# Kernel optimization log

Measured on AMD Instinct MI355X. Metric: run time of the kernel, lower is better.

## Reference

```python
import jax, jax.numpy as jnp
from jax import lax
import numpy as np

B, C, H, W = 32, 256, 56, 56
K = 3
EPS = 1e-5


def setup_inputs() -> dict:
    key = jax.random.key(0)
    k1, k2, k3, k4 = jax.random.split(key, 4)
    x = jax.random.normal(k1, (B, C, H, W), dtype=jnp.float32)
    # xavier_normal init for conv weight [C_out, C_in, K, K]
    fan_in = C * K * K
    fan_out = C * K * K
    std = float(np.sqrt(2.0 / (fan_in + fan_out)))
    w = jax.random.normal(k2, (C, C, K, K), dtype=jnp.float32) * std
    gamma = jnp.ones((C,), dtype=jnp.float32)
    beta = jnp.zeros((C,), dtype=jnp.float32)
    return {"x": x, "w": w, "gamma": gamma, "beta": beta}


def reference(x, w, gamma, beta):
    # --- Binarize (bi_act_method=0, bi_w_scale=1) ---
    bx = jnp.sign(x)                                   # activation sign
    wc = jnp.clip(w, -1.0, 1.0)                        # fp_weight.data.clamp_(-1,1)
    mean_val = jnp.mean(jnp.abs(wc))
    bw = jnp.sign(wc) * mean_val                       # sign(w) * mean(|w|)
    # --- float conv2d, stride 1, padding 1 ---
    out = lax.conv_general_dilated(
        bx, bw, window_strides=(1, 1), padding=[(1, 1), (1, 1)],
        dimension_numbers=("NCHW", "OIHW", "NCHW"))
    # --- identity shortcut (stride=1, C_in==C_out) ---
    out = out + x
    # --- BatchNorm2d (training-mode batch stats, affine) ---
    mean = jnp.mean(out, axis=(0, 2, 3), keepdims=True)
    var = jnp.var(out, axis=(0, 2, 3), keepdims=True)
    out = (out - mean) * lax.rsqrt(var + EPS)
    out = out * gamma[None, :, None, None] + beta[None, :, None, None]
    # --- ReLU ---
    return jax.nn.relu(out)
```

## Files before the change

### kernel.cpp

```cpp
#include <hip/hip_runtime.h>
#include <cstdint>

#define Bn   32
#define Cn   256
#define Hn   56
#define Wn   56
#define HWn  (Hn*Wn)
#define NPIX (Bn*HWn)
#define WELEMS (Cn*Cn*9)
#define EPSv 1e-5f

#define PR   58
#define PPLANE (PR*PR)

#define F_WPART 8
#define F_SUM   64
#define F_SQ    320
#define WPK_OFF  4096
#define WPK_BYTES WELEMS
#define ACT_OFF  (WPK_OFF + WPK_BYTES)
#define ACT_BYTES (Bn*PPLANE*Cn)

typedef int v4i __attribute__((ext_vector_type(4)));

#define GLOBAL_AS __attribute__((address_space(1)))
#define LDS_AS    __attribute__((address_space(3)))

__global__ void pack_all(const float* __restrict__ x,
                         const float* __restrict__ w,
                         float* __restrict__ wsf,
                         uint8_t* __restrict__ wpk,
                         uint8_t* __restrict__ act) {
    if (blockIdx.x < 392) {
        if (blockIdx.x < 2)
            wsf[F_SUM + blockIdx.x * 256 + threadIdx.x] = 0.0f;

        int v = blockIdx.x * 256 + threadIdx.x;
        if (v < 7296) {
            int b = v / 228;
            int r = v - b * 228;
            int y, xx;
            if (r < 58)       { y = 0;  xx = r; }
            else if (r < 116) { y = 57; xx = r - 58; }
            else { int r2 = r - 116; y = 1 + (r2 >> 1); xx = (r2 & 1) * 57; }
            uint4* d = (uint4*)(act + ((size_t)(b * PR + y) * PR + xx) * 256);
            uint4 z = make_uint4(0, 0, 0, 0);
            #pragma unroll
            for (int i = 0; i < 16; i++) d[i] = z;
        }
        int b = v / HWn;
        int p = v - b * HWn;
        int y = p / Wn;
        int xx = p - y * Wn;
        const float* xp = x + (size_t)b * Cn * HWn + p;
        int key = (xx + 1) & 15;
        uint32_t* dst = (uint32_t*)(act + ((size_t)(b * PR + (y + 1)) * PR + (xx + 1)) * 256);
        #pragma unroll
        for (int slot = 0; slot < 16; slot++) {
            uint32_t rr[4];
            #pragma unroll
            for (int cw = 0; cw < 4; cw++) {
                uint32_t r = 0;
                #pragma unroll
                for (int j = 0; j < 4; j++) {
                    uint32_t sgn = __float_as_uint(xp[(size_t)(slot * 16 + cw * 4 + j) * HWn]) >> 31;
                    r |= (sgn ? 0xFFu : 0x01u) << (j * 8);
                }
                rr[cw] = r;
            }
            *(uint4*)(dst + (size_t)((slot ^ key) * 4)) = make_uint4(rr[0], rr[1], rr[2], rr[3]);
        }
    } else {
        int u = (blockIdx.x - 392) * 256 + threadIdx.x;
        int co = u / 36;
        int kc = u - co * 36;
        int t  = kc >> 2;
        int s  = kc & 3;
        const float* wp = w + (size_t)co * 2304 + t;
        uint32_t* dst = (uint32_t*)(wpk + ((size_t)kc * 256 + co) * 64);
        float sabs = 0.0f;
        #pragma unroll
        for (int cw = 0; cw < 16; cw++) {
            uint32_t r = 0;
            #pragma unroll
            for (int j = 0; j < 4; j++) {
                int ci = s * 64 + cw * 4 + j;
                float wv = wp[(size_t)ci * 9];
                sabs += fminf(fabsf(wv), 1.0f);
                r |= ((__float_as_uint(wv) >> 31) ? 0xFFu : 0x01u) << (j * 8);
            }
            dst[cw] = r;
        }
        #pragma unroll
        for (int off = 32; off; off >>= 1) sabs += __shfl_down(sabs, off);
        __shared__ float sh[4];
        if ((threadIdx.x & 63) == 0) sh[threadIdx.x >> 6] = sabs;
        __syncthreads();
        if (threadIdx.x == 0)
            wsf[F_WPART + (blockIdx.x - 392)] = sh[0] + sh[1] + sh[2] + sh[3];
    }
}

__global__ __launch_bounds__(256, 2) void conv_mfma(
    const uint8_t* __restrict__ act, const uint8_t* __restrict__ wpk,
    const float* __restrict__ x, float* __restrict__ wsf,
    float* __restrict__ out) {
    __shared__ uint4 ldsv[3712];
    uint8_t* lds = (uint8_t*)ldsv;

    const int tid  = threadIdx.x;
    const int lane = tid & 63;
    const int wid  = tid >> 6;
    const int l15  = lane & 15;
    const int l4   = lane >> 4;

    const int bx = blockIdx.x;
    const int b  = bx / 28;
    const int y0 = (bx - b * 28) * 2;

    {
        const uint8_t* src = act + ((size_t)b * PR + y0) * PR * 256;
        #pragma unroll
        for (int j = 0; j < 15; j++) {
            int c = wid + j * 4;
            if (c < 58) {
                __builtin_amdgcn_global_load_lds(
                    (const GLOBAL_AS uint32_t*)(const void*)(src + c * 1024 + lane * 16),
                    (LDS_AS uint32_t*)(void*)(lds + c * 1024),
                    16, 0, 0);
            }
        }
    }

    const uint8_t* abase = wpk + (wid * 64 + l15) * 64 + l4 * 16;

    v4i af0[4], af1[4], af2[4], af3[4];
    #pragma unroll
    for (int mi = 0; mi < 4; mi++) {
        af0[mi] = *(const v4i*)(abase + (size_t)0 * 16384 + mi * 1024);
        af1[mi] = *(const v4i*)(abase + (size_t)1 * 16384 + mi * 1024);
        af2[mi] = *(const v4i*)(abase + (size_t)2 * 16384 + mi * 1024);
        af3[mi] = *(const v4i*)(abase + (size_t)3 * 16384 + mi * 1024);
    }

    int pixb[7], key[7];
    #pragma unroll
    for (int ni = 0; ni < 7; ni++) {
        int n  = ni * 16 + l15;
        int r_ = n / 56;
        int c_ = n - r_ * 56;
        pixb[ni] = (r_ * 58 + c_) * 256;
        key[ni]  = c_ & 15;
    }

    __syncthreads();

    v4i acc[4][7] = {};

#define STEP(S, AF)                                                            \
    {                                                                          \
        v4i bf[7];                                                             \
        _Pragma("unroll")                                                      \
        for (int ni = 0; ni < 7; ni++)                                         \
            bf[ni] = *(const v4i*)(lds + pixb[ni] +                            \
                                   ((((S) * 4 + l4) ^ key[ni]) << 4));         \
        _Pragma("unroll")                                                      \
        for (int ni = 0; ni < 7; ni++) {                                       \
            _Pragma("unroll")                                                  \
            for (int mi = 0; mi < 4; mi++)                                     \
                acc[mi][ni] = __builtin_amdgcn_mfma_i32_16x16x64_i8(           \
                    AF[mi], bf[ni], acc[mi][ni], 0, 0, 0);                     \
        }                                                                      \
        {                                                                      \
            int kcn = t4 + (S) + 4;                                            \
            kcn = kcn > 35 ? 35 : kcn;     \
            const uint8_t* ap = abase + (size_t)kcn * 16384;                   \
            _Pragma("unroll")                                                  \
            for (int mi = 0; mi < 4; mi++)                                     \
                AF[mi] = *(const v4i*)(ap + mi * 1024);                        \
        }                                                                      \
    }

    #pragma unroll 1
    for (int t = 0; t < 9; t++) {
        const int t4 = t * 4;
        STEP(0, af0)
        STEP(1, af1)
        STEP(2, af2)
        STEP(3, af3)
        const int wrap  = (t == 2 || t == 5);
        const int dtoff = (t == 8) ? 0 : (wrap ? 56 * 256 : 256);
        const int ddw   = (t == 8) ? 0 : (wrap ? -2 : 1);
        #pragma unroll
        for (int ni = 0; ni < 7; ni++) {
            pixb[ni] += dtoff;
            key[ni]   = (key[ni] + ddw) & 15;
        }
    }
#undef STEP

    float wabs = 0.0f;
    #pragma unroll
    for (int j = 0; j < 36; j++) wabs += wsf[F_WPART + j];
    const float mv = wabs * (1.0f / (float)WELEMS);

    const int co_w = wid * 64;
    const int pbase = b * (Cn * HWn) + y0 * 56;

    float ssum[4][4] = {}, ssq[4][4] = {};
    #pragma unroll
    for (int mi = 0; mi < 4; mi++) {
        #pragma unroll
        for (int ni = 0; ni < 7; ni++) {
            v4i a = acc[mi][ni];
            #pragma unroll
            for (int q = 0; q < 4; q++) {
                int co = co_w + mi * 16 + l4 * 4 + q;
                size_t idx = (size_t)pbase + (size_t)co * HWn + (ni * 16 + l15);
                float val = fmaf(mv, (float)a[q], x[idx]);
                out[idx] = val;
                ssum[mi][q] += val;
                ssq[mi][q]  += val * val;
            }
        }
    }
    #pragma unroll
    for (int mi = 0; mi < 4; mi++) {
        #pragma unroll
        for (int q = 0; q < 4; q++) {
            float s = ssum[mi][q], sq = ssq[mi][q];
            #pragma unroll
            for (int off = 1; off < 16; off <<= 1) {
                s  += __shfl_xor(s, off);
                sq += __shfl_xor(sq, off);
            }
            if (l15 == 0) {
                int co = co_w + mi * 16 + l4 * 4 + q;
                atomicAdd(&wsf[F_SUM + co], s);
                atomicAdd(&wsf[F_SQ  + co], sq);
            }
        }
    }
}

__global__ void epilogue_kernel(float* __restrict__ out,
                                const float* __restrict__ wsf,
                                const float* __restrict__ g,
                                const float* __restrict__ bt) {
    int plane = blockIdx.x;
    int c = plane & 255;
    const float n = (float)(Bn * HWn);
    float mean = wsf[F_SUM + c] / n;
    float var  = wsf[F_SQ + c] / n - mean * mean;
    float sc = g[c] * rsqrtf(var + EPSv);
    float sh = bt[c] - mean * sc;
    float4* o4 = (float4*)(out + (size_t)plane * HWn);
    for (int i = threadIdx.x; i < HWn / 4; i += 256) {
        float4 v = o4[i];
        v.x = fmaxf(fmaf(v.x, sc, sh), 0.0f);
        v.y = fmaxf(fmaf(v.y, sc, sh), 0.0f);
        v.z = fmaxf(fmaf(v.z, sc, sh), 0.0f);
        v.w = fmaxf(fmaf(v.w, sc, sh), 0.0f);
        o4[i] = v;
    }
}

extern "C" void kernel_launch(void* const* d_in, const int* in_sizes, int n_in,
                              void* d_out, int out_size, void* d_ws, size_t ws_size,
                              hipStream_t stream) {
    const float* x     = (const float*)d_in[0];
    const float* w     = (const float*)d_in[1];
    const float* gamma = (const float*)d_in[2];
    const float* beta  = (const float*)d_in[3];
    float* out = (float*)d_out;

    float*   wsf = (float*)d_ws;
    uint8_t* wpk = (uint8_t*)d_ws + WPK_OFF;
    uint8_t* act = (uint8_t*)d_ws + ACT_OFF;

    pack_all<<<dim3(428), dim3(256), 0, stream>>>(x, w, wsf, wpk, act);
    conv_mfma<<<dim3(896), dim3(256), 0, stream>>>(act, wpk, x, wsf, out);
    epilogue_kernel<<<dim3(Bn * Cn), dim3(256), 0, stream>>>(out, wsf, gamma, beta);
}
```

Baseline: 346.8 us.

## Split conv block into 8 waves, each handling half the pixel tiles

Doubles the conv block from 256 to 512 threads. Each pair of waves now shares one 64-output-channel group and splits its 7 pixel tiles into 4 and 3. Weight prefetch shrinks from four steps ahead to one step, which cuts per-thread registers (fewer accumulators and A fragments) and targets higher occupancy through launch bounds (512,4). In exchange, weight fragments are loaded twice per block, prefetch distance is shorter and latency may be exposed, and the 4/3 split leaves the two halves of each wave pair with unequal work.

```diff
diff --git a/kernel.cpp b/kernel.cpp
--- a/kernel.cpp
+++ b/kernel.cpp
@@ -101,7 +101,109 @@
     }
 }
 
-__global__ __launch_bounds__(256, 2) void conv_mfma(
+template<int NF>
+__device__ __forceinline__ void conv_body(
+    const uint8_t* lds, const uint8_t* abase,
+    const float* __restrict__ x, float* __restrict__ wsf,
+    float* __restrict__ out, float mv,
+    int f0, int l15, int l4, int co_w, int pbase) {
+
+    int pixb[NF], key[NF];
+    #pragma unroll
+    for (int ni = 0; ni < NF; ni++) {
+        int n  = (f0 + ni) * 16 + l15;
+        int r_ = n / 56;
+        int c_ = n - r_ * 56;
+        pixb[ni] = (r_ * 58 + c_) * 256;
+        key[ni]  = c_ & 15;
+    }
+
+    v4i af[4];
+    #pragma unroll
+    for (int mi = 0; mi < 4; mi++)
+        af[mi] = *(const v4i*)(abase + mi * 1024);
+
+    v4i acc[4][NF] = {};
+
+#define STEP(S)                                                                \
+    {                                                                          \
+        v4i bf[NF];                                                            \
+        _Pragma("unroll")                                                      \
+        for (int ni = 0; ni < NF; ni++)                                        \
+            bf[ni] = *(const v4i*)(lds + pixb[ni] +                            \
+                                   ((((S) * 4 + l4) ^ key[ni]) << 4));         \
+        _Pragma("unroll")                                                      \
+        for (int ni = 0; ni < NF; ni++) {                                      \
+            _Pragma("unroll")                                                  \
+            for (int mi = 0; mi < 4; mi++)                                     \
+                acc[mi][ni] = __builtin_amdgcn_mfma_i32_16x16x64_i8(           \
+                    af[mi], bf[ni], acc[mi][ni], 0, 0, 0);                     \
+        }                                                                      \
+        {                                                                      \
+            int kcn = t4 + (S) + 1;                                            \
+            kcn = kcn > 35 ? 35 : kcn;     \
+            const uint8_t* ap = abase + (size_t)kcn * 16384;                   \
+            _Pragma("unroll")                                                  \
+            for (int mi = 0; mi < 4; mi++)                                     \
+                af[mi] = *(const v4i*)(ap + mi * 1024);                        \
+        }                                                                      \
+    }
+
+    #pragma unroll 1
+    for (int t = 0; t < 9; t++) {
+        const int t4 = t * 4;
+        STEP(0)
+        STEP(1)
+        STEP(2)
+        STEP(3)
+        const int wrap  = (t == 2 || t == 5);
+        const int dtoff = (t == 8) ? 0 : (wrap ? 56 * 256 : 256);
+        const int ddw   = (t == 8) ? 0 : (wrap ? -2 : 1);
+        #pragma unroll
+        for (int ni = 0; ni < NF; ni++) {
+            pixb[ni] += dtoff;
+            key[ni]   = (key[ni] + ddw) & 15;
+        }
+    }
+#undef STEP
+
+    float ssum[4][4] = {}, ssq[4][4] = {};
+    #pragma unroll
+    for (int mi = 0; mi < 4; mi++) {
+        #pragma unroll
+        for (int ni = 0; ni < NF; ni++) {
+            v4i a = acc[mi][ni];
+            #pragma unroll
+            for (int q = 0; q < 4; q++) {
+                int co = co_w + mi * 16 + l4 * 4 + q;
+                size_t idx = (size_t)pbase + (size_t)co * HWn + ((f0 + ni) * 16 + l15);
+                float val = fmaf(mv, (float)a[q], x[idx]);
+                out[idx] = val;
+                ssum[mi][q] += val;
+                ssq[mi][q]  += val * val;
+            }
+        }
+    }
+    #pragma unroll
+    for (int mi = 0; mi < 4; mi++) {
+        #pragma unroll
+        for (int q = 0; q < 4; q++) {
+            float s = ssum[mi][q], sq = ssq[mi][q];
+            #pragma unroll
+            for (int off = 1; off < 16; off <<= 1) {
+                s  += __shfl_xor(s, off);
+                sq += __shfl_xor(sq, off);
+            }
+            if (l15 == 0) {
+                int co = co_w + mi * 16 + l4 * 4 + q;
+                atomicAdd(&wsf[F_SUM + co], s);
+                atomicAdd(&wsf[F_SQ  + co], sq);
+            }
+        }
+    }
+}
+
+__global__ __launch_bounds__(512, 4) void conv_mfma(
     const uint8_t* __restrict__ act, const uint8_t* __restrict__ wpk,
     const float* __restrict__ x, float* __restrict__ wsf,
     float* __restrict__ out) {
@@ -113,6 +215,8 @@
     const int wid  = tid >> 6;
     const int l15  = lane & 15;
     const int l4   = lane >> 4;
+    const int g    = wid >> 1;
+    const int h    = wid & 1;
 
     const int bx = blockIdx.x;
     const int b  = bx / 28;
@@ -121,8 +225,8 @@
     {
         const uint8_t* src = act + ((size_t)b * PR + y0) * PR * 256;
         #pragma unroll
-        for (int j = 0; j < 15; j++) {
-            int c = wid + j * 4;
+        for (int j = 0; j < 8; j++) {
+            int c = wid + j * 8;
             if (c < 58) {
                 __builtin_amdgcn_global_load_lds(
                     (const GLOBAL_AS uint32_t*)(const void*)(src + c * 1024 + lane * 16),
@@ -132,115 +236,21 @@
         }
     }
 
-    const uint8_t* abase = wpk + (wid * 64 + l15) * 64 + l4 * 16;
-
-    v4i af0[4], af1[4], af2[4], af3[4];
-    #pragma unroll
-    for (int mi = 0; mi < 4; mi++) {
-        af0[mi] = *(const v4i*)(abase + (size_t)0 * 16384 + mi * 1024);
-        af1[mi] = *(const v4i*)(abase + (size_t)1 * 16384 + mi * 1024);
-        af2[mi] = *(const v4i*)(abase + (size_t)2 * 16384 + mi * 1024);
-        af3[mi] = *(const v4i*)(abase + (size_t)3 * 16384 + mi * 1024);
-    }
-
-    int pixb[7], key[7];
-    #pragma unroll
-    for (int ni = 0; ni < 7; ni++) {
-        int n  = ni * 16 + l15;
-        int r_ = n / 56;
-        int c_ = n - r_ * 56;
-        pixb[ni] = (r_ * 58 + c_) * 256;
-        key[ni]  = c_ & 15;
-    }
-
-    __syncthreads();
-
-    v4i acc[4][7] = {};
-
-#define STEP(S, AF)                                                            \
-    {                                                                          \
-        v4i bf[7];                                                             \
-        _Pragma("unroll")                                                      \
-        for (int ni = 0; ni < 7; ni++)                                         \
-            bf[ni] = *(const v4i*)(lds + pixb[ni] +                            \
-                                   ((((S) * 4 + l4) ^ key[ni]) << 4));         \
-        _Pragma("unroll")                                                      \
-        for (int ni = 0; ni < 7; ni++) {                                       \
-            _Pragma("unroll")                                                  \
-            for (int mi = 0; mi < 4; mi++)                                     \
-                acc[mi][ni] = __builtin_amdgcn_mfma_i32_16x16x64_i8(           \
-                    AF[mi], bf[ni], acc[mi][ni], 0, 0, 0);                     \
-        }                                                                      \
-        {                                                                      \
-            int kcn = t4 + (S) + 4;                                            \
-            kcn = kcn > 35 ? 35 : kcn;     \
-            const uint8_t* ap = abase + (size_t)kcn * 16384;                   \
-            _Pragma("unroll")                                                  \
-            for (int mi = 0; mi < 4; mi++)                                     \
-                AF[mi] = *(const v4i*)(ap + mi * 1024);                        \
-        }                                                                      \
-    }
-
-    #pragma unroll 1
-    for (int t = 0; t < 9; t++) {
-        const int t4 = t * 4;
-        STEP(0, af0)
-        STEP(1, af1)
-        STEP(2, af2)
-        STEP(3, af3)
-        const int wrap  = (t == 2 || t == 5);
-        const int dtoff = (t == 8) ? 0 : (wrap ? 56 * 256 : 256);
-        const int ddw   = (t == 8) ? 0 : (wrap ? -2 : 1);
-        #pragma unroll
-        for (int ni = 0; ni < 7; ni++) {
-            pixb[ni] += dtoff;
-            key[ni]   = (key[ni] + ddw) & 15;
-        }
-    }
-#undef STEP
-
     float wabs = 0.0f;
     #pragma unroll
     for (int j = 0; j < 36; j++) wabs += wsf[F_WPART + j];
     const float mv = wabs * (1.0f / (float)WELEMS);
 
-    const int co_w = wid * 64;
+    const uint8_t* abase = wpk + (g * 64 + l15) * 64 + l4 * 16;
+    const int co_w  = g * 64;
     const int pbase = b * (Cn * HWn) + y0 * 56;
 
-    float ssum[4][4] = {}, ssq[4][4] = {};
-    #pragma unroll
-    for (int mi = 0; mi < 4; mi++) {
-        #pragma unroll
-        for (int ni = 0; ni < 7; ni++) {
-            v4i a = acc[mi][ni];
-            #pragma unroll
-            for (int q = 0; q < 4; q++) {
-                int co = co_w + mi * 16 + l4 * 4 + q;
-                size_t idx = (size_t)pbase + (size_t)co * HWn + (ni * 16 + l15);
-                float val = fmaf(mv, (float)a[q], x[idx]);
-                out[idx] = val;
-                ssum[mi][q] += val;
-                ssq[mi][q]  += val * val;
-            }
-        }
-    }
-    #pragma unroll
-    for (int mi = 0; mi < 4; mi++) {
-        #pragma unroll
-        for (int q = 0; q < 4; q++) {
-            float s = ssum[mi][q], sq = ssq[mi][q];
-            #pragma unroll
-            for (int off = 1; off < 16; off <<= 1) {
-                s  += __shfl_xor(s, off);
-                sq += __shfl_xor(sq, off);
-            }
-            if (l15 == 0) {
-                int co = co_w + mi * 16 + l4 * 4 + q;
-                atomicAdd(&wsf[F_SUM + co], s);
-                atomicAdd(&wsf[F_SQ  + co], sq);
-            }
-        }
-    }
+    __syncthreads();
+
+    if (h == 0)
+        conv_body<4>(lds, abase, x, wsf, out, mv, 0, l15, l4, co_w, pbase);
+    else
+        conv_body<3>(lds, abase, x, wsf, out, mv, 4, l15, l4, co_w, pbase);
 }
 
 __global__ void epilogue_kernel(float* __restrict__ out,
@@ -279,6 +289,6 @@
     uint8_t* act = (uint8_t*)d_ws + ACT_OFF;
 
     pack_all<<<dim3(428), dim3(256), 0, stream>>>(x, w, wsf, wpk, act);
-    conv_mfma<<<dim3(896), dim3(256), 0, stream>>>(act, wpk, x, wsf, out);
+    conv_mfma<<<dim3(896), dim3(512), 0, stream>>>(act, wpk, x, wsf, out);
     epilogue_kernel<<<dim3(Bn * Cn), dim3(256), 0, stream>>>(out, wsf, gamma, beta);
 }
```

After: 480.0 us. +38.4%, slower.
